# Performance work log

Hardware: AMD Instinct MI355X
Metric: run time of the kernel (lower is better)

Reference implementation:

```python
import jax, jax.numpy as jnp
import numpy as np

DIM = 768
H = 12        # query heads
HKV = 4       # kv heads
G = H // HKV  # GQA group size
HD = 64       # head dim
CAP = 50.0    # soft cap (Gemma-2 style)
EPS = 1e-6
SCALE = HD ** -0.5
B, T, S = 1, 128, 256


def setup_inputs() -> dict:
    key = jax.random.key(0)
    ks = jax.random.split(key, 5)
    s = DIM ** -0.5
    x = jax.random.normal(ks[0], (B, T, S, DIM), jnp.float32)
    Wq = jax.random.normal(ks[1], (DIM, H * HD), jnp.float32) * s
    Wk = jax.random.normal(ks[2], (DIM, HKV * HD), jnp.float32) * s
    Wv = jax.random.normal(ks[3], (DIM, HKV * HD), jnp.float32) * s
    Wo = jax.random.normal(ks[4], (H * HD, DIM), jnp.float32) * s
    q_norm_w = jnp.ones((HD,), jnp.float32)
    k_norm_w = jnp.ones((HD,), jnp.float32)
    return {"x": x, "Wq": Wq, "Wk": Wk, "Wv": Wv, "Wo": Wo,
            "q_norm_w": q_norm_w, "k_norm_w": k_norm_w}


def _rmsnorm(x, w):
    # x: (..., HD)
    return x * jax.lax.rsqrt(jnp.mean(x * x, axis=-1, keepdims=True) + EPS) * w


def reference(x, Wq, Wk, Wv, Wo, q_norm_w, k_norm_w):
    b, t, s, d = x.shape
    n = b * s
    # fold spatial into batch: temporal attention per spatial position
    xf = x.transpose(0, 2, 1, 3).reshape(n, t, d)             # (N, T, D)
    q = (xf @ Wq).reshape(n, t, H, HD).transpose(0, 2, 1, 3)   # (N, H, T, hd)
    k = (xf @ Wk).reshape(n, t, HKV, HD).transpose(0, 2, 1, 3) # (N, Hkv, T, hd)
    v = (xf @ Wv).reshape(n, t, HKV, HD).transpose(0, 2, 1, 3)
    # QKNorm (per-head RMSNorm on head_dim)
    q = _rmsnorm(q, q_norm_w)
    k = _rmsnorm(k, k_norm_w)
    # GQA without materializing repeated K/V: split q heads into (Hkv, G)
    # (repeat_interleave maps query head h -> kv head h // G, matching kv*G+g)
    qg = q.reshape(n, HKV, G, t, HD)
    attn = jnp.einsum('bkgtd,bksd->bkgts', qg, k) * SCALE      # (N, Hkv, G, T, T)
    attn = CAP * jnp.tanh(attn / CAP)                          # soft cap
    causal = jnp.triu(jnp.ones((t, t), bool), 1)               # True above diag
    attn = jnp.where(causal, -jnp.inf, attn)
    attn = jax.nn.softmax(attn, axis=-1)
    out = jnp.einsum('bkgts,bksd->bkgtd', attn, v)             # (N, Hkv, G, T, hd)
    out = out.reshape(n, H, t, HD).transpose(0, 2, 1, 3).reshape(n, t, H * HD)
    out = out @ Wo                                             # (N, T, D)
    return out.reshape(b, s, t, d).transpose(0, 2, 1, 3)        # (B, T, S, D)
```

## Files before the change

kernel.cpp:

```cpp
#include <hip/hip_runtime.h>
#include <stdint.h>
#include <stddef.h>

#define DIM 768
#define NH  12
#define NKV 4
#define HD  64
#define TT  128
#define NS  256

typedef __attribute__((ext_vector_type(8))) short bf16x8;
typedef __attribute__((ext_vector_type(4))) float f32x4;
typedef __attribute__((ext_vector_type(4))) unsigned int u32x4;
typedef __attribute__((ext_vector_type(2))) unsigned int u32x2;

__device__ __forceinline__ unsigned short f2bf(float f) {
  union { float f; unsigned int u; } v; v.f = f;
  return (unsigned short)((v.u + 0x7FFFu + ((v.u >> 16) & 1u)) >> 16);
}

__device__ __forceinline__ void gload_lds16(const void* g, void* l) {
  __builtin_amdgcn_global_load_lds(
      (const __attribute__((address_space(1))) unsigned int*)g,
      (__attribute__((address_space(3))) unsigned int*)l, 16, 0, 0);
}

__global__ __launch_bounds__(256)
void prep_kernel(const float* __restrict__ x, const float* __restrict__ Wq,
                 const float* __restrict__ Wk, const float* __restrict__ Wv,
                 const float* __restrict__ Wo, unsigned short* __restrict__ Wt,
                 unsigned short* __restrict__ WoT, unsigned short* __restrict__ xb) {
  const int b = blockIdx.x, tid = threadIdx.x;
  if (b < 6144) {
    int idx = b * 256 + tid;
    const int n1 = 1280 * DIM;
    if (idx < n1) {
      int c = idx / DIM, kk = idx - c * DIM;
      float v;
      if (c < 768)       v = Wq[kk * 768 + c];
      else if (c < 1024) v = Wk[kk * 256 + (c - 768)];
      else               v = Wv[kk * 256 + (c - 1024)];
      Wt[idx] = f2bf(v);
    } else {
      int i2 = idx - n1;
      int c = i2 / DIM, kk = i2 - c * DIM;
      WoT[i2] = f2bf(Wo[kk * 768 + c]);
    }
  } else {
    int g = (b - 6144) * 256 + tid;
    int r = g / 192;
    int k = g - r * 192;
    int t = r >> 8, n = r & 255;
    f32x4 f = *reinterpret_cast<const f32x4*>(x + (size_t)g * 4);
    u32x2 pk;
    pk[0] = (unsigned)f2bf(f[0]) | ((unsigned)f2bf(f[1]) << 16);
    pk[1] = (unsigned)f2bf(f[2]) | ((unsigned)f2bf(f[3]) << 16);
    *reinterpret_cast<u32x2*>(xb + (size_t)((n << 7) + t) * DIM + k * 4) = pk;
  }
}

__global__ __launch_bounds__(512, 2)
void qkv_kernel(const unsigned short* __restrict__ xb, const float* __restrict__ qnw,
                const float* __restrict__ knw, const unsigned short* __restrict__ Wt,
                unsigned short* __restrict__ qb, unsigned short* __restrict__ kb,
                unsigned short* __restrict__ vTb) {
  extern __shared__ unsigned short lds[];
  const int b = blockIdx.x;
  const int x8 = b & 7, idx = b >> 3;
  const int cbt = idx % 5;
  const int n   = (idx / 5) * 8 + x8;
  const int tid = threadIdx.x;
  const int wave = tid >> 6, lane = tid & 63;
  const int cl = lane & 15, rowg = lane >> 4;
  const int wmw = wave >> 2, wn = wave & 3;
  const int l8 = lane >> 3, s8 = lane & 7;
  const unsigned short* asrc = xb + (size_t)(n * TT + l8) * DIM + (s8 ^ l8) * 8;
  const unsigned short* bsrc = Wt + (size_t)(cbt * 256 + l8) * DIM + (s8 ^ l8) * 8;
  const int swzr = (cl & 7) << 4;
  f32x4 acc[4][4] = {};

#define QKV_STAGE(buf, ko)                                                  \
  {                                                                         \
    unsigned short* Ad = lds + (buf) * 24576;                               \
    unsigned short* Bd = Ad + 8192;                                         \
    _Pragma("unroll")                                                       \
    for (int i = 0; i < 2; ++i) {                                           \
      const int rr = i * 64 + wave * 8;                                     \
      gload_lds16(asrc + (size_t)rr * DIM + (ko), Ad + rr * 64);            \
    }                                                                       \
    _Pragma("unroll")                                                       \
    for (int i = 0; i < 4; ++i) {                                           \
      const int rr = i * 64 + wave * 8;                                     \
      gload_lds16(bsrc + (size_t)rr * DIM + (ko), Bd + rr * 64);            \
    }                                                                       \
  }

  QKV_STAGE(0, 0);
  __syncthreads();
  for (int kt = 0; kt < 12; ++kt) {
    if (kt < 11) QKV_STAGE((kt + 1) & 1, (kt + 1) * 64);
    const char* Ab = (const char*)(lds + (kt & 1) * 24576);
    const char* Bb = Ab + 16384;
    #pragma unroll
    for (int ks = 0; ks < 2; ++ks) {
      bf16x8 a[4], bb[4];
      #pragma unroll
      for (int m = 0; m < 4; ++m)
        a[m] = *(const bf16x8*)(Ab + (wmw * 64 + m * 16 + cl) * 128 + ((ks * 64 + rowg * 16) ^ swzr));
      #pragma unroll
      for (int nn = 0; nn < 4; ++nn)
        bb[nn] = *(const bf16x8*)(Bb + (wn * 64 + nn * 16 + cl) * 128 + ((ks * 64 + rowg * 16) ^ swzr));
      #pragma unroll
      for (int m = 0; m < 4; ++m)
        #pragma unroll
        for (int nn = 0; nn < 4; ++nn)
          acc[m][nn] = __builtin_amdgcn_mfma_f32_16x16x32_bf16(a[m], bb[nn], acc[m][nn], 0, 0, 0);
    }
    __syncthreads();
  }
#undef QKV_STAGE

  if (cbt == 4) {
    const int kv = wn;
    unsigned short* dst = vTb + (size_t)((n * NKV + kv) * HD) * TT;
    #pragma unroll
    for (int m = 0; m < 4; ++m) {
      const int tb = wmw * 64 + m * 16 + rowg * 4;
      #pragma unroll
      for (int nn = 0; nn < 4; ++nn) {
        const int d = nn * 16 + cl;
        u32x2 pk;
        pk[0] = (unsigned)f2bf(acc[m][nn][0]) | ((unsigned)f2bf(acc[m][nn][1]) << 16);
        pk[1] = (unsigned)f2bf(acc[m][nn][2]) | ((unsigned)f2bf(acc[m][nn][3]) << 16);
        *reinterpret_cast<u32x2*>(dst + (size_t)d * TT + tb) = pk;
      }
    }
  } else {
    const int isq = (cbt < 3);
    const float* nw = isq ? qnw : knw;
    float wfrag[4];
    #pragma unroll
    for (int nn = 0; nn < 4; ++nn) wfrag[nn] = nw[nn * 16 + cl];
    const float rs = isq ? 0.125f : 1.0f;
    unsigned short* dst;
    if (isq) { const int hh = cbt * 4 + wn; dst = qb + (size_t)(n * NH + hh) * TT * HD; }
    else     { const int kv = wn;           dst = kb + (size_t)(n * NKV + kv) * TT * HD; }
    #pragma unroll
    for (int m = 0; m < 4; ++m) {
      #pragma unroll
      for (int j = 0; j < 4; ++j) {
        const int t = wmw * 64 + m * 16 + rowg * 4 + j;
        float ss = 0.f;
        #pragma unroll
        for (int nn = 0; nn < 4; ++nn) { float v = acc[m][nn][j]; ss += v * v; }
        #pragma unroll
        for (int dlt = 1; dlt < 16; dlt <<= 1) ss += __shfl_xor(ss, dlt);
        const float r = rsqrtf(ss * (1.f / 64.f) + 1e-6f) * rs;
        #pragma unroll
        for (int nn = 0; nn < 4; ++nn)
          dst[(size_t)t * HD + nn * 16 + cl] = f2bf(acc[m][nn][j] * r * wfrag[nn]);
      }
    }
  }
}

__global__ __launch_bounds__(256)
void attn_kernel(const unsigned short* __restrict__ qb, const unsigned short* __restrict__ kb,
                 const unsigned short* __restrict__ vTb, unsigned short* __restrict__ ab) {
  extern __shared__ char smem[];
  unsigned short (*Ks)[72]   = reinterpret_cast<unsigned short (*)[72]>(smem);
  unsigned short (*Vts)[136] = reinterpret_cast<unsigned short (*)[136]>(smem + 18432);
  unsigned short (*Pl)[136]  = reinterpret_cast<unsigned short (*)[136]>(smem + 35840);
  const int b = blockIdx.x;
  const int x8 = b & 7, idx = b >> 3;
  const int kv = idx & 3;
  const int n  = (idx >> 2) * 8 + x8;
  const int tid = threadIdx.x, wave = tid >> 6, lane = tid & 63;
  const int cl = lane & 15, rowg = lane >> 4;

  const unsigned short* ksrc = kb + (size_t)(n * NKV + kv) * TT * HD;
  const unsigned short* vsrc = vTb + (size_t)(n * NKV + kv) * HD * TT;
  #pragma unroll
  for (int i = 0; i < 4; ++i) {
    int c = tid + 256 * i, r = c >> 3, seg = c & 7;
    *reinterpret_cast<u32x4*>(&Ks[r][seg * 8]) = *reinterpret_cast<const u32x4*>(ksrc + c * 8);
  }
  #pragma unroll
  for (int i = 0; i < 4; ++i) {
    int c = tid + 256 * i, r = c >> 4, seg = c & 15;
    *reinterpret_cast<u32x4*>(&Vts[r][seg * 8]) = *reinterpret_cast<const u32x4*>(vsrc + c * 8);
  }
  __syncthreads();

  for (int hh = 0; hh < 3; ++hh) {
    const int h = kv * 3 + hh;
    const unsigned short* qsrc = qb + (size_t)(n * NH + h) * TT * HD;
    f32x4 sc[2][8] = {};
    #pragma unroll
    for (int ks = 0; ks < 2; ++ks) {
      bf16x8 a[2], bbf[8];
      #pragma unroll
      for (int m = 0; m < 2; ++m)
        a[m] = *reinterpret_cast<const bf16x8*>(
            qsrc + (size_t)(wave * 32 + m * 16 + cl) * HD + ks * 32 + rowg * 8);
      #pragma unroll
      for (int nn = 0; nn < 8; ++nn)
        bbf[nn] = *reinterpret_cast<const bf16x8*>(&Ks[nn * 16 + cl][ks * 32 + rowg * 8]);
      #pragma unroll
      for (int m = 0; m < 2; ++m)
        #pragma unroll
        for (int nn = 0; nn < 8; ++nn)
          sc[m][nn] = __builtin_amdgcn_mfma_f32_16x16x32_bf16(a[m], bbf[nn], sc[m][nn], 0, 0, 0);
    }
    #pragma unroll
    for (int m = 0; m < 2; ++m) {
      #pragma unroll
      for (int j = 0; j < 4; ++j) {
        const int rowv = wave * 32 + m * 16 + rowg * 4 + j;
        float e8[8];
        float sum = 0.f;
        #pragma unroll
        for (int nn = 0; nn < 8; ++nn) {
          float s = sc[m][nn][j];
          const float z2 = s * s * 4.0e-4f;
          s = s * (27.f + z2) * __builtin_amdgcn_rcpf(27.f + 9.f * z2);
          float e = __expf(s - 50.f);
          if (nn * 16 + cl > rowv) e = 0.f;
          e8[nn] = e;
          sum += e;
        }
        #pragma unroll
        for (int d = 1; d < 16; d <<= 1) sum += __shfl_xor(sum, d);
        const float inv = __builtin_amdgcn_rcpf(sum);
        #pragma unroll
        for (int nn = 0; nn < 8; ++nn)
          Pl[rowv][nn * 16 + cl] = f2bf(e8[nn] * inv);
      }
    }
    f32x4 o[2][4] = {};
    #pragma unroll
    for (int ks = 0; ks < 4; ++ks) {
      bf16x8 a[2], bbf[4];
      #pragma unroll
      for (int m = 0; m < 2; ++m)
        a[m] = *reinterpret_cast<const bf16x8*>(&Pl[wave * 32 + m * 16 + cl][ks * 32 + rowg * 8]);
      #pragma unroll
      for (int nn = 0; nn < 4; ++nn)
        bbf[nn] = *reinterpret_cast<const bf16x8*>(&Vts[nn * 16 + cl][ks * 32 + rowg * 8]);
      #pragma unroll
      for (int m = 0; m < 2; ++m)
        #pragma unroll
        for (int nn = 0; nn < 4; ++nn)
          o[m][nn] = __builtin_amdgcn_mfma_f32_16x16x32_bf16(a[m], bbf[nn], o[m][nn], 0, 0, 0);
    }
    unsigned short* dst = ab + (size_t)n * TT * DIM + h * HD;
    #pragma unroll
    for (int m = 0; m < 2; ++m)
      #pragma unroll
      for (int j = 0; j < 4; ++j) {
        int t = wave * 32 + m * 16 + rowg * 4 + j;
        #pragma unroll
        for (int nn = 0; nn < 4; ++nn)
          dst[(size_t)t * DIM + nn * 16 + cl] = f2bf(o[m][nn][j]);
      }
  }
}

__global__ __launch_bounds__(512, 2)
void out_kernel(const unsigned short* __restrict__ ab, const unsigned short* __restrict__ WoT,
                float* __restrict__ out) {
  extern __shared__ unsigned short lds[];
  const int b = blockIdx.x;
  const int x8 = b & 7, idx = b >> 3;
  const int cbt = idx % 3;
  const int n   = (idx / 3) * 8 + x8;
  const int tid = threadIdx.x;
  const int wave = tid >> 6, lane = tid & 63;
  const int cl = lane & 15, rowg = lane >> 4;
  const int wmw = wave >> 2, wn = wave & 3;
  const int l8 = lane >> 3, s8 = lane & 7;
  const unsigned short* asrc = ab  + (size_t)(n * TT + l8) * DIM + (s8 ^ l8) * 8;
  const unsigned short* bsrc = WoT + (size_t)(cbt * 256 + l8) * DIM + (s8 ^ l8) * 8;
  const int swzr = (cl & 7) << 4;
  f32x4 acc[4][4] = {};

#define OUT_STAGE(buf, ko)                                                  \
  {                                                                         \
    unsigned short* Ad = lds + (buf) * 24576;                               \
    unsigned short* Bd = Ad + 8192;                                         \
    _Pragma("unroll")                                                       \
    for (int i = 0; i < 2; ++i) {                                           \
      const int rr = i * 64 + wave * 8;                                     \
      gload_lds16(asrc + (size_t)rr * DIM + (ko), Ad + rr * 64);            \
    }                                                                       \
    _Pragma("unroll")                                                       \
    for (int i = 0; i < 4; ++i) {                                           \
      const int rr = i * 64 + wave * 8;                                     \
      gload_lds16(bsrc + (size_t)rr * DIM + (ko), Bd + rr * 64);            \
    }                                                                       \
  }

  OUT_STAGE(0, 0);
  __syncthreads();
  for (int kt = 0; kt < 12; ++kt) {
    if (kt < 11) OUT_STAGE((kt + 1) & 1, (kt + 1) * 64);
    const char* Ab = (const char*)(lds + (kt & 1) * 24576);
    const char* Bb = Ab + 16384;
    #pragma unroll
    for (int ks = 0; ks < 2; ++ks) {
      bf16x8 a[4], bb[4];
      #pragma unroll
      for (int m = 0; m < 4; ++m)
        a[m] = *(const bf16x8*)(Ab + (wmw * 64 + m * 16 + cl) * 128 + ((ks * 64 + rowg * 16) ^ swzr));
      #pragma unroll
      for (int nn = 0; nn < 4; ++nn)
        bb[nn] = *(const bf16x8*)(Bb + (wn * 64 + nn * 16 + cl) * 128 + ((ks * 64 + rowg * 16) ^ swzr));
      #pragma unroll
      for (int m = 0; m < 4; ++m)
        #pragma unroll
        for (int nn = 0; nn < 4; ++nn)
          acc[m][nn] = __builtin_amdgcn_mfma_f32_16x16x32_bf16(a[m], bb[nn], acc[m][nn], 0, 0, 0);
    }
    __syncthreads();
  }
#undef OUT_STAGE
  #pragma unroll
  for (int m = 0; m < 4; ++m)
    #pragma unroll
    for (int j = 0; j < 4; ++j) {
      int t = wmw * 64 + m * 16 + rowg * 4 + j;
      #pragma unroll
      for (int nn = 0; nn < 4; ++nn)
        out[(size_t)(t * NS + n) * DIM + cbt * 256 + wn * 64 + nn * 16 + cl] = acc[m][nn][j];
    }
}

extern "C" void kernel_launch(void* const* d_in, const int* in_sizes, int n_in,
                              void* d_out, int out_size, void* d_ws, size_t ws_size,
                              hipStream_t stream) {
  const float* x   = (const float*)d_in[0];
  const float* Wq  = (const float*)d_in[1];
  const float* Wk  = (const float*)d_in[2];
  const float* Wv  = (const float*)d_in[3];
  const float* Wo  = (const float*)d_in[4];
  const float* qnw = (const float*)d_in[5];
  const float* knw = (const float*)d_in[6];
  (void)in_sizes; (void)n_in; (void)out_size;

  char* ws = (char*)d_ws;
  unsigned short* Wt  = (unsigned short*)(ws + 0);
  unsigned short* WoT = (unsigned short*)(ws + 1966080);
  unsigned short* qb  = (unsigned short*)(ws + 3145728);
  unsigned short* kb  = (unsigned short*)(ws + 53477376);
  unsigned short* vTb = (unsigned short*)(ws + 70254592);
  unsigned short* ab  = (unsigned short*)(ws + 87031808);
  unsigned short* xb  = ab;
  if (ws_size < 137363456) return;

  hipFuncSetAttribute(reinterpret_cast<const void*>(qkv_kernel),
                      hipFuncAttributeMaxDynamicSharedMemorySize, 98304);
  hipFuncSetAttribute(reinterpret_cast<const void*>(out_kernel),
                      hipFuncAttributeMaxDynamicSharedMemorySize, 98304);
  hipFuncSetAttribute(reinterpret_cast<const void*>(attn_kernel),
                      hipFuncAttributeMaxDynamicSharedMemorySize, 70656);

  prep_kernel<<<30720, 256, 0, stream>>>(x, Wq, Wk, Wv, Wo, Wt, WoT, xb);
  qkv_kernel<<<1280, 512, 98304, stream>>>(xb, qnw, knw, Wt, qb, kb, vTb);
  attn_kernel<<<1024, 256, 70656, stream>>>(qb, kb, vTb, ab);
  out_kernel<<<768, 512, 98304, stream>>>(ab, WoT, (float*)d_out);
}
```

Measured before the change: 211.6 us.

## Fuse fp32-to-bf16 conversion of x into the QKV GEMM load path

Removes the separate pass that converts and transposes x to bf16. The QKV GEMM now streams fp32 x directly into LDS with a swizzled layout and packs it to bf16 when loading MFMA fragments. This avoids writing and rereading an intermediate bf16 copy of x. In exchange, the A-tile global traffic doubles and LDS per block grows to 128 KB, which may reduce occupancy. Wave priority is also raised around the MFMA block.

```diff
diff --git a/kernel.cpp b/kernel.cpp
--- a/kernel.cpp
+++ b/kernel.cpp
@@ -26,41 +26,27 @@
 }
 
 __global__ __launch_bounds__(256)
-void prep_kernel(const float* __restrict__ x, const float* __restrict__ Wq,
-                 const float* __restrict__ Wk, const float* __restrict__ Wv,
-                 const float* __restrict__ Wo, unsigned short* __restrict__ Wt,
-                 unsigned short* __restrict__ WoT, unsigned short* __restrict__ xb) {
-  const int b = blockIdx.x, tid = threadIdx.x;
-  if (b < 6144) {
-    int idx = b * 256 + tid;
-    const int n1 = 1280 * DIM;
-    if (idx < n1) {
-      int c = idx / DIM, kk = idx - c * DIM;
-      float v;
-      if (c < 768)       v = Wq[kk * 768 + c];
-      else if (c < 1024) v = Wk[kk * 256 + (c - 768)];
-      else               v = Wv[kk * 256 + (c - 1024)];
-      Wt[idx] = f2bf(v);
-    } else {
-      int i2 = idx - n1;
-      int c = i2 / DIM, kk = i2 - c * DIM;
-      WoT[i2] = f2bf(Wo[kk * 768 + c]);
-    }
+void prep_kernel(const float* __restrict__ Wq, const float* __restrict__ Wk,
+                 const float* __restrict__ Wv, const float* __restrict__ Wo,
+                 unsigned short* __restrict__ Wt, unsigned short* __restrict__ WoT) {
+  int idx = blockIdx.x * 256 + threadIdx.x;
+  const int n1 = 1280 * DIM;
+  if (idx < n1) {
+    int c = idx / DIM, kk = idx - c * DIM;
+    float v;
+    if (c < 768)       v = Wq[kk * 768 + c];
+    else if (c < 1024) v = Wk[kk * 256 + (c - 768)];
+    else               v = Wv[kk * 256 + (c - 1024)];
+    Wt[idx] = f2bf(v);
   } else {
-    int g = (b - 6144) * 256 + tid;
-    int r = g / 192;
-    int k = g - r * 192;
-    int t = r >> 8, n = r & 255;
-    f32x4 f = *reinterpret_cast<const f32x4*>(x + (size_t)g * 4);
-    u32x2 pk;
-    pk[0] = (unsigned)f2bf(f[0]) | ((unsigned)f2bf(f[1]) << 16);
-    pk[1] = (unsigned)f2bf(f[2]) | ((unsigned)f2bf(f[3]) << 16);
-    *reinterpret_cast<u32x2*>(xb + (size_t)((n << 7) + t) * DIM + k * 4) = pk;
+    int i2 = idx - n1;
+    int c = i2 / DIM, kk = i2 - c * DIM;
+    WoT[i2] = f2bf(Wo[kk * 768 + c]);
   }
 }
 
 __global__ __launch_bounds__(512, 2)
-void qkv_kernel(const unsigned short* __restrict__ xb, const float* __restrict__ qnw,
+void qkv_kernel(const float* __restrict__ x, const float* __restrict__ qnw,
                 const float* __restrict__ knw, const unsigned short* __restrict__ Wt,
                 unsigned short* __restrict__ qb, unsigned short* __restrict__ kb,
                 unsigned short* __restrict__ vTb) {
@@ -74,51 +60,72 @@
   const int cl = lane & 15, rowg = lane >> 4;
   const int wmw = wave >> 2, wn = wave & 3;
   const int l8 = lane >> 3, s8 = lane & 7;
-  const unsigned short* asrc = xb + (size_t)(n * TT + l8) * DIM + (s8 ^ l8) * 8;
   const unsigned short* bsrc = Wt + (size_t)(cbt * 256 + l8) * DIM + (s8 ^ l8) * 8;
   const int swzr = (cl & 7) << 4;
+  const int arow_off = lane >> 4;
+  const int aslot    = lane & 15;
   f32x4 acc[4][4] = {};
 
-#define QKV_STAGE(buf, ko)                                                  \
-  {                                                                         \
-    unsigned short* Ad = lds + (buf) * 24576;                               \
-    unsigned short* Bd = Ad + 8192;                                         \
-    _Pragma("unroll")                                                       \
-    for (int i = 0; i < 2; ++i) {                                           \
-      const int rr = i * 64 + wave * 8;                                     \
-      gload_lds16(asrc + (size_t)rr * DIM + (ko), Ad + rr * 64);            \
-    }                                                                       \
-    _Pragma("unroll")                                                       \
-    for (int i = 0; i < 4; ++i) {                                           \
-      const int rr = i * 64 + wave * 8;                                     \
-      gload_lds16(bsrc + (size_t)rr * DIM + (ko), Bd + rr * 64);            \
-    }                                                                       \
-  }
-
-  QKV_STAGE(0, 0);
+#define STAGE_AF(buf, ko)                                                    \
+  _Pragma("unroll")                                                          \
+  for (int i = 0; i < 4; ++i) {                                              \
+    const int r0 = i * 32 + wave * 4;                                        \
+    const int rr = r0 + arow_off;                                            \
+    const int seg = aslot ^ (rr & 7);                                        \
+    gload_lds16(x + (size_t)(rr * NS + n) * DIM + (ko) + seg * 4,            \
+                (char*)lds + (buf) * 32768 + r0 * 256);                      \
+  }
+#define STAGE_B(buf, ko)                                                     \
+  {                                                                          \
+    unsigned short* Bd = lds + 32768 + (buf) * 16384;                        \
+    _Pragma("unroll")                                                        \
+    for (int i = 0; i < 4; ++i) {                                            \
+      const int rr = i * 64 + wave * 8;                                      \
+      gload_lds16(bsrc + (size_t)rr * DIM + (ko), Bd + rr * 64);             \
+    }                                                                        \
+  }
+#define LDA_F(ks, m, dst)                                                    \
+  {                                                                          \
+    const int R = wmw * 64 + (m) * 16 + cl;                                  \
+    const int sb = (ks) * 8 + rowg * 2;                                      \
+    const char* base_ = (const char*)lds + (kt & 1) * 32768 + R * 256;       \
+    f32x4 lo = *(const f32x4*)(base_ + ((sb ^ (R & 7)) << 4));               \
+    f32x4 hi = *(const f32x4*)(base_ + (((sb + 1) ^ (R & 7)) << 4));         \
+    u32x4 pk_;                                                               \
+    asm("v_cvt_pk_bf16_f32 %0, %1, %2" : "=v"(pk_[0]) : "v"(lo[0]), "v"(lo[1])); \
+    asm("v_cvt_pk_bf16_f32 %0, %1, %2" : "=v"(pk_[1]) : "v"(lo[2]), "v"(lo[3])); \
+    asm("v_cvt_pk_bf16_f32 %0, %1, %2" : "=v"(pk_[2]) : "v"(hi[0]), "v"(hi[1])); \
+    asm("v_cvt_pk_bf16_f32 %0, %1, %2" : "=v"(pk_[3]) : "v"(hi[2]), "v"(hi[3])); \
+    dst = *(bf16x8*)&pk_;                                                    \
+  }
+
+  STAGE_AF(0, 0);
+  STAGE_B(0, 0);
   __syncthreads();
   for (int kt = 0; kt < 12; ++kt) {
-    if (kt < 11) QKV_STAGE((kt + 1) & 1, (kt + 1) * 64);
-    const char* Ab = (const char*)(lds + (kt & 1) * 24576);
-    const char* Bb = Ab + 16384;
+    if (kt < 11) { STAGE_AF((kt + 1) & 1, (kt + 1) * 64); STAGE_B((kt + 1) & 1, (kt + 1) * 64); }
+    const char* Bb = (const char*)(lds + 32768 + (kt & 1) * 16384);
     #pragma unroll
     for (int ks = 0; ks < 2; ++ks) {
       bf16x8 a[4], bb[4];
       #pragma unroll
-      for (int m = 0; m < 4; ++m)
-        a[m] = *(const bf16x8*)(Ab + (wmw * 64 + m * 16 + cl) * 128 + ((ks * 64 + rowg * 16) ^ swzr));
+      for (int m = 0; m < 4; ++m) LDA_F(ks, m, a[m]);
       #pragma unroll
       for (int nn = 0; nn < 4; ++nn)
         bb[nn] = *(const bf16x8*)(Bb + (wn * 64 + nn * 16 + cl) * 128 + ((ks * 64 + rowg * 16) ^ swzr));
+      __builtin_amdgcn_s_setprio(1);
       #pragma unroll
       for (int m = 0; m < 4; ++m)
         #pragma unroll
         for (int nn = 0; nn < 4; ++nn)
           acc[m][nn] = __builtin_amdgcn_mfma_f32_16x16x32_bf16(a[m], bb[nn], acc[m][nn], 0, 0, 0);
+      __builtin_amdgcn_s_setprio(0);
     }
     __syncthreads();
   }
-#undef QKV_STAGE
+#undef STAGE_AF
+#undef STAGE_B
+#undef LDA_F
 
   if (cbt == 4) {
     const int kv = wn;
@@ -354,18 +361,17 @@
   unsigned short* kb  = (unsigned short*)(ws + 53477376);
   unsigned short* vTb = (unsigned short*)(ws + 70254592);
   unsigned short* ab  = (unsigned short*)(ws + 87031808);
-  unsigned short* xb  = ab;
   if (ws_size < 137363456) return;
 
   hipFuncSetAttribute(reinterpret_cast<const void*>(qkv_kernel),
-                      hipFuncAttributeMaxDynamicSharedMemorySize, 98304);
+                      hipFuncAttributeMaxDynamicSharedMemorySize, 131072);
   hipFuncSetAttribute(reinterpret_cast<const void*>(out_kernel),
                       hipFuncAttributeMaxDynamicSharedMemorySize, 98304);
   hipFuncSetAttribute(reinterpret_cast<const void*>(attn_kernel),
                       hipFuncAttributeMaxDynamicSharedMemorySize, 70656);
 
-  prep_kernel<<<30720, 256, 0, stream>>>(x, Wq, Wk, Wv, Wo, Wt, WoT, xb);
-  qkv_kernel<<<1280, 512, 98304, stream>>>(xb, qnw, knw, Wt, qb, kb, vTb);
+  prep_kernel<<<6144, 256, 0, stream>>>(Wq, Wk, Wv, Wo, Wt, WoT);
+  qkv_kernel<<<1280, 512, 131072, stream>>>(x, qnw, knw, Wt, qb, kb, vTb);
   attn_kernel<<<1024, 256, 70656, stream>>>(qb, kb, vTb, ab);
   out_kernel<<<768, 512, 98304, stream>>>(ab, WoT, (float*)d_out);
 }
```

After: 229.7 us. 1.09x slower.
